# Optimization experiments

Hardware: AMD Instinct MI355X
Metric: run time of the kernel (lower is better)

Reference implementation:

```python
import jax, jax.numpy as jnp
import numpy as np

HADAMARD_DIM = 4096  # power of 2 -> had_rem_dim is None, rem_dim = 1


def _fwht(x):
    """Fast Walsh-Hadamard transform along last dim (natural/Sylvester order).

    x: [B, n] with n a power of 2. Returns x @ H_n (unnormalized).
    Mirrors QuaRot's recursive butterfly: at each stage, pairs are split into
    (a+b) and (a-b) halves. log2(n) stages, each O(n) work per row.
    """
    bsz, n = x.shape
    steps = int(np.log2(n))
    u = x[:, :, None]  # [B, n, 1]
    m = n
    for _ in range(steps):  # fixed-trip loop over log2(n) stages, jit-friendly
        u = u.reshape(bsz, m // 2, 2, -1)
        a = u[:, :, 0, :]
        b = u[:, :, 1, :]
        u = jnp.concatenate([a + b, a - b], axis=-1)  # [B, m//2, 2k]
        m //= 2
    return u.reshape(bsz, n)


def matmul_hadU(x):
    """QuaRot matmul_hadU for power-of-2 dim: normalized FWHT, 1/sqrt(n)."""
    n = x.shape[-1]
    flat = x.reshape(-1, n)
    out = _fwht(flat) * (1.0 / np.sqrt(n))
    return out.reshape(x.shape).astype(x.dtype)


def setup_inputs() -> dict:
    key = jax.random.key(0)
    x = jax.random.normal(key, (8192, HADAMARD_DIM), dtype=jnp.float32)
    return {"x": x}


def reference(x):
    # FWHT.forward: x -> matmul_hadU_cuda(x, None, 1) -> cast back to x.dtype
    return matmul_hadU(x)
```

## Files before the change

kernel.cpp:

```cpp
#include <hip/hip_runtime.h>


#define N        4096
#define THREADS  256

__global__ __launch_bounds__(THREADS)
void FWHT_83476984365427_kernel(const float* __restrict__ x,
                                float* __restrict__ out,
                                int nrows) {
    const int wid = blockIdx.x * (THREADS / 64) + (threadIdx.x >> 6);
    if (wid >= nrows) return;
    const int l = threadIdx.x & 63;

    const float* __restrict__ xr  = x   + (size_t)wid * N;
    float* __restrict__       otr = out + (size_t)wid * N;

    float v[64];

#pragma unroll
    for (int i = 0; i < 16; i++) {
        float4 f = *(const float4*)(xr + i * 256 + l * 4);
        v[4 * i + 0] = f.x;
        v[4 * i + 1] = f.y;
        v[4 * i + 2] = f.z;
        v[4 * i + 3] = f.w;
    }

#pragma unroll
    for (int s = 1; s < 4; s <<= 1) {
#pragma unroll
        for (int k = 0; k < 64; k++) {
            if ((k & s) == 0) {
                float a = v[k];
                float b = v[k + s];
                v[k]     = a + b;
                v[k + s] = a - b;
            }
        }
    }

#pragma unroll
    for (int m = 1; m < 64; m <<= 1) {
        const float sgn = (l & m) ? -1.0f : 1.0f;
#pragma unroll
        for (int r = 0; r < 64; r++) {
            float p = __shfl_xor(v[r], m, 64);
            v[r] = fmaf(sgn, v[r], p);
        }
    }

#pragma unroll
    for (int s = 4; s < 64; s <<= 1) {
#pragma unroll
        for (int k = 0; k < 64; k++) {
            if ((k & s) == 0) {
                float a = v[k];
                float b = v[k + s];
                v[k]     = a + b;
                v[k + s] = a - b;
            }
        }
    }

    const float scale = 1.0f / 64.0f;
#pragma unroll
    for (int i = 0; i < 16; i++) {
        float4 f;
        f.x = v[4 * i + 0] * scale;
        f.y = v[4 * i + 1] * scale;
        f.z = v[4 * i + 2] * scale;
        f.w = v[4 * i + 3] * scale;
        *(float4*)(otr + i * 256 + l * 4) = f;
    }
}

extern "C" void kernel_launch(void* const* d_in, const int* in_sizes, int n_in,
                              void* d_out, int out_size, void* d_ws, size_t ws_size,
                              hipStream_t stream) {
    (void)n_in; (void)d_ws; (void)ws_size; (void)out_size;
    const float* x = (const float*)d_in[0];
    float* out = (float*)d_out;
    const int nrows = in_sizes[0] / N;
    const int wpb = THREADS / 64;
    dim3 grid((nrows + wpb - 1) / wpb);
    dim3 block(THREADS);
    FWHT_83476984365427_kernel<<<grid, block, 0, stream>>>(x, out, nrows);
}
```

Measured before the change: 234.2 us.

## Process four rows per wave with double-buffered register prefetch

Each wave now handles four rows and keeps two 64-float register buffers, so it loads the next row while the FWHT of the current row runs. The goal is to hide global memory latency behind the shuffle and butterfly work within a single wave. Holding 128 live floats raises register pressure and cuts occupancy. The grid is also four times smaller, which may leave compute units underused and reduce the number of independent waves available for latency hiding.

```diff
diff --git a/kernel.cpp b/kernel.cpp
--- a/kernel.cpp
+++ b/kernel.cpp
@@ -3,42 +3,20 @@
 
 #define N        4096
 #define THREADS  256
+#define RPW      4
 
-__global__ __launch_bounds__(THREADS)
-void FWHT_83476984365427_kernel(const float* __restrict__ x,
-                                float* __restrict__ out,
-                                int nrows) {
-    const int wid = blockIdx.x * (THREADS / 64) + (threadIdx.x >> 6);
-    if (wid >= nrows) return;
-    const int l = threadIdx.x & 63;
-
-    const float* __restrict__ xr  = x   + (size_t)wid * N;
-    float* __restrict__       otr = out + (size_t)wid * N;
-
-    float v[64];
-
-#pragma unroll
-    for (int i = 0; i < 16; i++) {
-        float4 f = *(const float4*)(xr + i * 256 + l * 4);
-        v[4 * i + 0] = f.x;
-        v[4 * i + 1] = f.y;
-        v[4 * i + 2] = f.z;
-        v[4 * i + 3] = f.w;
-    }
-
+__device__ __forceinline__ void fwht_row(float v[64], const int l) {
 #pragma unroll
     for (int s = 1; s < 4; s <<= 1) {
 #pragma unroll
         for (int k = 0; k < 64; k++) {
             if ((k & s) == 0) {
-                float a = v[k];
-                float b = v[k + s];
-                v[k]     = a + b;
+                float a = v[k], b = v[k + s];
+                v[k] = a + b;
                 v[k + s] = a - b;
             }
         }
     }
-
 #pragma unroll
     for (int m = 1; m < 64; m <<= 1) {
         const float sgn = (l & m) ? -1.0f : 1.0f;
@@ -48,30 +26,80 @@
             v[r] = fmaf(sgn, v[r], p);
         }
     }
-
 #pragma unroll
     for (int s = 4; s < 64; s <<= 1) {
 #pragma unroll
         for (int k = 0; k < 64; k++) {
             if ((k & s) == 0) {
-                float a = v[k];
-                float b = v[k + s];
-                v[k]     = a + b;
+                float a = v[k], b = v[k + s];
+                v[k] = a + b;
                 v[k + s] = a - b;
             }
         }
     }
+}
 
+__global__ __launch_bounds__(THREADS)
+void FWHT_83476984365427_kernel(const float* __restrict__ x,
+                                float* __restrict__ out,
+                                int nrows) {
+    const int wid = blockIdx.x * (THREADS / 64) + (threadIdx.x >> 6);
+    const int l   = threadIdx.x & 63;
+    const int r0  = wid * RPW;
+    if (r0 >= nrows) return;
+
+    float va[64], vb[64];
     const float scale = 1.0f / 64.0f;
-#pragma unroll
-    for (int i = 0; i < 16; i++) {
-        float4 f;
-        f.x = v[4 * i + 0] * scale;
-        f.y = v[4 * i + 1] * scale;
-        f.z = v[4 * i + 2] * scale;
-        f.w = v[4 * i + 3] * scale;
-        *(float4*)(otr + i * 256 + l * 4) = f;
+
+#define LOADROW(v_, row_)                                                  \
+    {                                                                      \
+        const float* __restrict__ xr_ = x + (size_t)(row_) * N;            \
+        _Pragma("unroll")                                                  \
+        for (int i = 0; i < 16; i++) {                                     \
+            float4 f = *(const float4*)(xr_ + i * 256 + l * 4);            \
+            v_[4 * i + 0] = f.x; v_[4 * i + 1] = f.y;                      \
+            v_[4 * i + 2] = f.z; v_[4 * i + 3] = f.w;                      \
+        }                                                                  \
     }
+
+#define STOREROW(v_, row_)                                                 \
+    {                                                                      \
+        float* __restrict__ or_ = out + (size_t)(row_) * N;                \
+        _Pragma("unroll")                                                  \
+        for (int i = 0; i < 16; i++) {                                     \
+            float4 f;                                                      \
+            f.x = v_[4 * i + 0] * scale; f.y = v_[4 * i + 1] * scale;      \
+            f.z = v_[4 * i + 2] * scale; f.w = v_[4 * i + 3] * scale;      \
+            *(float4*)(or_ + i * 256 + l * 4) = f;                         \
+        }                                                                  \
+    }
+
+    if (r0 + RPW <= nrows) {
+        LOADROW(va, r0 + 0);
+        LOADROW(vb, r0 + 1);
+
+        fwht_row(va, l);
+        STOREROW(va, r0 + 0);
+        LOADROW(va, r0 + 2);
+
+        fwht_row(vb, l);
+        STOREROW(vb, r0 + 1);
+        LOADROW(vb, r0 + 3);
+
+        fwht_row(va, l);
+        STOREROW(va, r0 + 2);
+
+        fwht_row(vb, l);
+        STOREROW(vb, r0 + 3);
+    } else {
+        for (int r = r0; r < nrows; r++) {
+            LOADROW(va, r);
+            fwht_row(va, l);
+            STOREROW(va, r);
+        }
+    }
+#undef LOADROW
+#undef STOREROW
 }
 
 extern "C" void kernel_launch(void* const* d_in, const int* in_sizes, int n_in,
@@ -81,8 +109,9 @@
     const float* x = (const float*)d_in[0];
     float* out = (float*)d_out;
     const int nrows = in_sizes[0] / N;
-    const int wpb = THREADS / 64;
-    dim3 grid((nrows + wpb - 1) / wpb);
+    const int waves = (nrows + RPW - 1) / RPW;
+    const int wpb   = THREADS / 64;
+    dim3 grid((waves + wpb - 1) / wpb);
     dim3 block(THREADS);
     FWHT_83476984365427_kernel<<<grid, block, 0, stream>>>(x, out, nrows);
 }
```

Result: slower. 242.8 us (+3.7%).
